# Kernel tuning notes

Measured on AMD Instinct MI355X. Metric: run time of the kernel, lower is better.

The kernel has to match this reference:

```python
import jax, jax.numpy as jnp
import numpy as np

B, T, C, H = 4, 2048, 1024, 16
HS = C // H  # head size = 64

def setup_inputs() -> dict:
    key = jax.random.key(0)
    ks = jax.random.split(key, 3)
    x = jax.random.normal(ks[0], (B, T, C), dtype=jnp.float32)
    w_attn = jax.random.normal(ks[1], (C, 3 * C), dtype=jnp.float32) * (1.0 / np.sqrt(C))
    b_attn = jnp.zeros((3 * C,), dtype=jnp.float32)
    w_proj = jax.random.normal(ks[2], (C, C), dtype=jnp.float32) * (1.0 / np.sqrt(C))
    b_proj = jnp.zeros((C,), dtype=jnp.float32)
    return {"x": x, "w_attn": w_attn, "b_attn": b_attn, "w_proj": w_proj, "b_proj": b_proj}

def reference(x, w_attn, b_attn, w_proj, b_proj):
    b, t, c = x.shape
    qkv = x @ w_attn + b_attn                       # [B,T,3C]
    q, k, v = jnp.split(qkv, 3, axis=2)             # each [B,T,C]
    # [B,T,C] -> [B,H,T,HS]
    q = q.reshape(b, t, H, HS).transpose(0, 2, 1, 3)
    k = k.reshape(b, t, H, HS).transpose(0, 2, 1, 3)
    v = v.reshape(b, t, H, HS).transpose(0, 2, 1, 3)
    scale = 1.0 / np.sqrt(HS)
    att = jnp.einsum('bhqd,bhkd->bhqk', q, k) * scale   # [B,H,T,T]
    causal = jnp.tril(jnp.ones((t, t), dtype=bool))
    att = jnp.where(causal[None, None, :, :], att, -jnp.inf)
    att = jax.nn.softmax(att, axis=-1)
    y = jnp.einsum('bhqk,bhkd->bhqd', att, v)           # [B,H,T,HS]
    y = y.transpose(0, 2, 1, 3).reshape(b, t, c)        # [B,T,C]
    return y @ w_proj + b_proj
```

## Files before the change

### kernel.cpp

```cpp
#include <hip/hip_runtime.h>
#include <hip/hip_bf16.h>

#define B_ 4
#define T_ 2048
#define C_ 1024
#define H_ 16
#define HS_ 64
#define M_ (B_*T_)
#define QSCALE 0.18033688011112042f

typedef __bf16 bf16_t;
typedef bf16_t bf16x8 __attribute__((ext_vector_type(8)));
typedef float f32x4 __attribute__((ext_vector_type(4)));
typedef unsigned short ushort_t;

__device__ __forceinline__ unsigned short f2bf(float f) {
    __hip_bfloat16 h = __float2bfloat16(f);
    return __builtin_bit_cast(unsigned short, h);
}

__device__ __forceinline__ void glds16(const void* g, void* l) {
    __builtin_amdgcn_global_load_lds((const __attribute__((address_space(1))) void*)g,
                                     (__attribute__((address_space(3))) void*)l, 16, 0, 0);
}

__launch_bounds__(256)
__global__ void cvt_x(const float* __restrict__ in, ushort_t* __restrict__ out) {
    int i = blockIdx.x * 256 + threadIdx.x;
    const float4* p = (const float4*)in;
    float4 a = p[i * 2], b = p[i * 2 + 1];
    ushort4 o0, o1;
    o0.x = f2bf(a.x); o0.y = f2bf(a.y); o0.z = f2bf(a.z); o0.w = f2bf(a.w);
    o1.x = f2bf(b.x); o1.y = f2bf(b.y); o1.z = f2bf(b.z); o1.w = f2bf(b.w);
    *(ushort4*)&out[i * 8] = o0;
    *(ushort4*)&out[i * 8 + 4] = o1;
}

__launch_bounds__(256)
__global__ void transpose_cvt(const float* __restrict__ w, ushort_t* __restrict__ wT,
                              int K, int N) {
    __shared__ ushort_t Ts[64][72];
    const int n0 = blockIdx.x * 64, k0 = blockIdx.y * 64;
    const int t = threadIdx.x, r = t >> 2, cq = t & 3;
    #pragma unroll
    for (int j = 0; j < 4; j++) {
        float4 v = *(const float4*)&w[(size_t)(k0 + r) * N + n0 + cq * 16 + j * 4];
        ushort4 o;
        o.x = f2bf(v.x); o.y = f2bf(v.y); o.z = f2bf(v.z); o.w = f2bf(v.w);
        *(ushort4*)&Ts[r][cq * 16 + j * 4] = o;
    }
    __syncthreads();
    #pragma unroll
    for (int j = 0; j < 4; j++) {
        ushort4 o;
        o.x = Ts[cq * 16 + j * 4 + 0][r];
        o.y = Ts[cq * 16 + j * 4 + 1][r];
        o.z = Ts[cq * 16 + j * 4 + 2][r];
        o.w = Ts[cq * 16 + j * 4 + 3][r];
        *(ushort4*)&wT[(size_t)(n0 + r) * K + k0 + cq * 16 + j * 4] = o;
    }
}

__launch_bounds__(256)
__global__ void qkv_gemm(const ushort_t* __restrict__ xb, const ushort_t* __restrict__ wT,
                         const float* __restrict__ bias,
                         ushort_t* __restrict__ qw, ushort_t* __restrict__ kw,
                         ushort_t* __restrict__ vt) {
    const int K = C_;
    __shared__ ushort_t As[2][128 * 32];
    __shared__ ushort_t Bs[2][128 * 32];
    const int tid = threadIdx.x, lane = tid & 63, wid = tid >> 6;
    const int cl = lane & 15, gl = lane >> 4;
    const int waveM = wid >> 1, waveN = wid & 1;
    const int m0 = blockIdx.y * 128, n0 = blockIdx.x * 128;
    const int srow = tid >> 2, scq = tid & 3;
    const int gsw = scq ^ ((srow >> 1) & 3);
    const int asw = 8 * (gl ^ ((cl >> 1) & 3));

    f32x4 acc[4][4];
    #pragma unroll
    for (int mf = 0; mf < 4; mf++)
        #pragma unroll
        for (int nf = 0; nf < 4; nf++) acc[mf][nf] = (f32x4)0.0f;

    #pragma unroll
    for (int i = 0; i < 2; i++) {
        int row = srow + i * 64;
        glds16(&xb[(size_t)(m0 + row) * K + gsw * 8], &As[0][row * 32 + scq * 8]);
        glds16(&wT[(size_t)(n0 + row) * K + gsw * 8], &Bs[0][row * 32 + scq * 8]);
    }
    __syncthreads();

    int cur = 0;
    for (int kk = 0; kk < K; kk += 32) {
        if (kk + 32 < K) {
            #pragma unroll
            for (int i = 0; i < 2; i++) {
                int row = srow + i * 64;
                glds16(&xb[(size_t)(m0 + row) * K + kk + 32 + gsw * 8], &As[cur ^ 1][row * 32 + scq * 8]);
                glds16(&wT[(size_t)(n0 + row) * K + kk + 32 + gsw * 8], &Bs[cur ^ 1][row * 32 + scq * 8]);
            }
        }
        bf16x8 a[4], b[4];
        #pragma unroll
        for (int mf = 0; mf < 4; mf++)
            a[mf] = *(bf16x8*)&As[cur][(waveM * 64 + mf * 16 + cl) * 32 + asw];
        #pragma unroll
        for (int nf = 0; nf < 4; nf++)
            b[nf] = *(bf16x8*)&Bs[cur][(waveN * 64 + nf * 16 + cl) * 32 + asw];
        #pragma unroll
        for (int mf = 0; mf < 4; mf++)
            #pragma unroll
            for (int nf = 0; nf < 4; nf++)
                acc[mf][nf] = __builtin_amdgcn_mfma_f32_16x16x32_bf16(a[mf], b[nf], acc[mf][nf], 0, 0, 0);
        __syncthreads();
        cur ^= 1;
    }
    const int secb = n0 >> 10;
    #pragma unroll
    for (int mf = 0; mf < 4; mf++)
        #pragma unroll
        for (int nf = 0; nf < 4; nf++)
            #pragma unroll
            for (int r = 0; r < 4; r++) {
                int rg = m0 + waveM * 64 + mf * 16 + 4 * gl + r;
                int cg = n0 + waveN * 64 + nf * 16 + cl;
                float val = acc[mf][nf][r] + bias[cg];
                int cc = cg & 1023;
                int h = cc >> 6, hs = cc & 63;
                int bb = rg >> 11, tq = rg & 2047;
                if (secb == 0)
                    qw[(((size_t)(bb * H_ + h)) * T_ + tq) * HS_ + hs] = f2bf(val * QSCALE);
                else if (secb == 1)
                    kw[(((size_t)(bb * H_ + h)) * T_ + tq) * HS_ + hs] = f2bf(val);
                else
                    vt[(((size_t)(bb * H_ + h)) * HS_ + hs) * T_ + tq] = f2bf(val);
            }
}

__launch_bounds__(512, 4)
__global__ void attn_mfma(const ushort_t* __restrict__ qw,
                          const ushort_t* __restrict__ kw,
                          const ushort_t* __restrict__ vt,
                          ushort_t* __restrict__ yw) {
    __shared__ ushort_t Ks[128][72];
    __shared__ ushort_t Vts[64][136];
    __shared__ ushort_t Ps[8][16][136];
    const int tid = threadIdx.x, lane = tid & 63, wid = tid >> 6;
    const int cl = lane & 15, gl = lane >> 4;
    const int qp = blockIdx.x;
    const int bh = blockIdx.y;
    const size_t base = (size_t)bh * T_ * HS_;
    const int bq = bh >> 4, h = bh & 15;
    const int srow = tid >> 3, scq = tid & 7;

    for (int half = 0; half < 2; half++) {
        const int qt = half ? (15 - qp) : qp;
        const int q0 = qt * 128 + wid * 16;
        const int ntiles = qt + 1;

        bf16x8 qf[2];
        #pragma unroll
        for (int kh = 0; kh < 2; kh++)
            qf[kh] = *(const bf16x8*)&qw[base + (size_t)(q0 + cl) * HS_ + kh * 32 + 8 * gl];

        f32x4 o_acc[4];
        #pragma unroll
        for (int dn = 0; dn < 4; dn++) o_acc[dn] = (f32x4)0.0f;
        float m_ = -INFINITY, l_ = 0.f;

        bf16x8 kpre[2], vpre[2], knew[2], vnew[2];
        kpre[0] = *(const bf16x8*)&kw[base + (size_t)srow * HS_ + scq * 8];
        kpre[1] = *(const bf16x8*)&kw[base + (size_t)(64 + srow) * HS_ + scq * 8];
        vpre[0] = *(const bf16x8*)&vt[base + (size_t)srow * T_ + scq * 8];
        vpre[1] = *(const bf16x8*)&vt[base + (size_t)srow * T_ + 64 + scq * 8];

        for (int kt = 0; kt < ntiles; kt++) {
            __syncthreads();
            if (kt + 1 < ntiles) {
                knew[0] = *(const bf16x8*)&kw[base + (size_t)((kt + 1) * 128 + srow) * HS_ + scq * 8];
                knew[1] = *(const bf16x8*)&kw[base + (size_t)((kt + 1) * 128 + 64 + srow) * HS_ + scq * 8];
                vnew[0] = *(const bf16x8*)&vt[base + (size_t)srow * T_ + (kt + 1) * 128 + scq * 8];
                vnew[1] = *(const bf16x8*)&vt[base + (size_t)srow * T_ + (kt + 1) * 128 + 64 + scq * 8];
            }
            *(bf16x8*)&Ks[srow][scq * 8] = kpre[0];
            *(bf16x8*)&Ks[64 + srow][scq * 8] = kpre[1];
            *(bf16x8*)&Vts[srow][scq * 8] = vpre[0];
            *(bf16x8*)&Vts[srow][scq * 8 + 64] = vpre[1];
            __syncthreads();

            {
                const bool full = (kt * 128 + 127 <= q0);

                f32x4 st[8];
                #pragma unroll
                for (int kn = 0; kn < 8; kn++) {
                    bf16x8 kf0 = *(bf16x8*)&Ks[kn * 16 + cl][8 * gl];
                    bf16x8 kf1 = *(bf16x8*)&Ks[kn * 16 + cl][32 + 8 * gl];
                    f32x4 t0 = (f32x4)0.0f;
                    t0 = __builtin_amdgcn_mfma_f32_16x16x32_bf16(kf0, qf[0], t0, 0, 0, 0);
                    st[kn] = __builtin_amdgcn_mfma_f32_16x16x32_bf16(kf1, qf[1], t0, 0, 0, 0);
                }
                if (!full) {
                    const int qg = q0 + cl;
                    #pragma unroll
                    for (int kn = 0; kn < 8; kn++)
                        #pragma unroll
                        for (int r = 0; r < 4; r++) {
                            int kv = kt * 128 + kn * 16 + 4 * gl + r;
                            if (kv > qg) st[kn][r] = -INFINITY;
                        }
                }

                float pmax = st[0][0];
                #pragma unroll
                for (int kn = 0; kn < 8; kn++)
                    #pragma unroll
                    for (int r = 0; r < 4; r++) pmax = fmaxf(pmax, st[kn][r]);
                if (!__all(pmax <= m_ + 8.0f)) {
                    float mx = pmax;
                    mx = fmaxf(mx, __shfl_xor(mx, 16));
                    mx = fmaxf(mx, __shfl_xor(mx, 32));
                    float nm = fmaxf(m_, mx);
                    float al = exp2f(m_ - nm);
                    l_ *= al;
                    #pragma unroll
                    for (int r = 0; r < 4; r++) {
                        float ag = __shfl(al, 4 * gl + r);
                        #pragma unroll
                        for (int dn = 0; dn < 4; dn++) o_acc[dn][r] *= ag;
                    }
                    m_ = nm;
                }

                float ps = 0.f;
                #pragma unroll
                for (int kn = 0; kn < 8; kn++) {
                    float p0 = exp2f(st[kn][0] - m_);
                    float p1 = exp2f(st[kn][1] - m_);
                    float p2 = exp2f(st[kn][2] - m_);
                    float p3 = exp2f(st[kn][3] - m_);
                    ps += (p0 + p1) + (p2 + p3);
                    unsigned lo, hi;
                    asm("v_cvt_pk_bf16_f32 %0, %1, %2" : "=v"(lo) : "v"(p0), "v"(p1));
                    asm("v_cvt_pk_bf16_f32 %0, %1, %2" : "=v"(hi) : "v"(p2), "v"(p3));
                    uint2 wv; wv.x = lo; wv.y = hi;
                    *(uint2*)&Ps[wid][cl][kn * 16 + 4 * gl] = wv;
                }
                l_ += ps;

                bf16x8 pf[4];
                #pragma unroll
                for (int ks = 0; ks < 4; ks++)
                    pf[ks] = *(bf16x8*)&Ps[wid][cl][ks * 32 + 8 * gl];
                #pragma unroll
                for (int dn = 0; dn < 4; dn++)
                    #pragma unroll
                    for (int ks = 0; ks < 4; ks++) {
                        bf16x8 vf = *(bf16x8*)&Vts[dn * 16 + cl][ks * 32 + 8 * gl];
                        o_acc[dn] = __builtin_amdgcn_mfma_f32_16x16x32_bf16(pf[ks], vf, o_acc[dn], 0, 0, 0);
                    }
            }
            #pragma unroll
            for (int i = 0; i < 2; i++) { kpre[i] = knew[i]; vpre[i] = vnew[i]; }
        }

        float ls = l_;
        ls += __shfl_xor(ls, 16);
        ls += __shfl_xor(ls, 32);
        float linv = 1.0f / ls;
        #pragma unroll
        for (int r = 0; r < 4; r++) {
            float lr = __shfl(linv, 4 * gl + r);
            int qg = q0 + 4 * gl + r;
            #pragma unroll
            for (int dn = 0; dn < 4; dn++) {
                int d = dn * 16 + cl;
                yw[((size_t)(bq * T_ + qg)) * C_ + h * HS_ + d] = f2bf(o_acc[dn][r] * lr);
            }
        }
    }
}

__launch_bounds__(256)
__global__ void proj_gemm(const ushort_t* __restrict__ y, const ushort_t* __restrict__ wT,
                          const float* __restrict__ bias, float* __restrict__ out) {
    const int K = C_, N = C_;
    __shared__ ushort_t As[2][128 * 32];
    __shared__ ushort_t Bs[2][128 * 32];
    const int tid = threadIdx.x, lane = tid & 63, wid = tid >> 6;
    const int cl = lane & 15, gl = lane >> 4;
    const int waveM = wid >> 1, waveN = wid & 1;
    const int m0 = blockIdx.y * 128, n0 = blockIdx.x * 128;
    const int srow = tid >> 2, scq = tid & 3;
    const int gsw = scq ^ ((srow >> 1) & 3);
    const int asw = 8 * (gl ^ ((cl >> 1) & 3));

    f32x4 acc[4][4];
    #pragma unroll
    for (int mf = 0; mf < 4; mf++)
        #pragma unroll
        for (int nf = 0; nf < 4; nf++) acc[mf][nf] = (f32x4)0.0f;

    #pragma unroll
    for (int i = 0; i < 2; i++) {
        int row = srow + i * 64;
        glds16(&y[(size_t)(m0 + row) * K + gsw * 8], &As[0][row * 32 + scq * 8]);
        glds16(&wT[(size_t)(n0 + row) * K + gsw * 8], &Bs[0][row * 32 + scq * 8]);
    }
    __syncthreads();

    int cur = 0;
    for (int kk = 0; kk < K; kk += 32) {
        if (kk + 32 < K) {
            #pragma unroll
            for (int i = 0; i < 2; i++) {
                int row = srow + i * 64;
                glds16(&y[(size_t)(m0 + row) * K + kk + 32 + gsw * 8], &As[cur ^ 1][row * 32 + scq * 8]);
                glds16(&wT[(size_t)(n0 + row) * K + kk + 32 + gsw * 8], &Bs[cur ^ 1][row * 32 + scq * 8]);
            }
        }
        bf16x8 a[4], b[4];
        #pragma unroll
        for (int mf = 0; mf < 4; mf++)
            a[mf] = *(bf16x8*)&As[cur][(waveM * 64 + mf * 16 + cl) * 32 + asw];
        #pragma unroll
        for (int nf = 0; nf < 4; nf++)
            b[nf] = *(bf16x8*)&Bs[cur][(waveN * 64 + nf * 16 + cl) * 32 + asw];
        #pragma unroll
        for (int mf = 0; mf < 4; mf++)
            #pragma unroll
            for (int nf = 0; nf < 4; nf++)
                acc[mf][nf] = __builtin_amdgcn_mfma_f32_16x16x32_bf16(a[mf], b[nf], acc[mf][nf], 0, 0, 0);
        __syncthreads();
        cur ^= 1;
    }
    #pragma unroll
    for (int mf = 0; mf < 4; mf++)
        #pragma unroll
        for (int nf = 0; nf < 4; nf++)
            #pragma unroll
            for (int r = 0; r < 4; r++) {
                int rg = m0 + waveM * 64 + mf * 16 + 4 * gl + r;
                int cg = n0 + waveN * 64 + nf * 16 + cl;
                out[(size_t)rg * N + cg] = acc[mf][nf][r] + bias[cg];
            }
}

extern "C" void kernel_launch(void* const* d_in, const int* in_sizes, int n_in,
                              void* d_out, int out_size, void* d_ws, size_t ws_size,
                              hipStream_t stream) {
    const float* x      = (const float*)d_in[0];
    const float* w_attn = (const float*)d_in[1];
    const float* b_attn = (const float*)d_in[2];
    const float* w_proj = (const float*)d_in[3];
    const float* b_proj = (const float*)d_in[4];
    float* out = (float*)d_out;

    const size_t E = (size_t)M_ * C_;
    ushort_t* qw  = (ushort_t*)d_ws;
    ushort_t* kw  = qw + E;
    ushort_t* vt  = kw + E;
    ushort_t* xy  = vt + E;
    ushort_t* wat = xy + E;
    ushort_t* wpt = vt;

    cvt_x<<<dim3(4096), 256, 0, stream>>>(x, xy);
    transpose_cvt<<<dim3(48, 16), 256, 0, stream>>>(w_attn, wat, C_, 3 * C_);
    qkv_gemm<<<dim3(24, 64), 256, 0, stream>>>(xy, wat, b_attn, qw, kw, vt);
    attn_mfma<<<dim3(8, 64), 512, 0, stream>>>(qw, kw, vt, xy);
    transpose_cvt<<<dim3(16, 16), 256, 0, stream>>>(w_proj, wpt, C_, C_);
    proj_gemm<<<dim3(8, 64), 256, 0, stream>>>(xy, wpt, b_proj, out);
}
```

Baseline: 297.7 us.

## Triple-buffer GEMM k-loop with vmcnt waits, swizzle block order, prioritize attention MFMAs

```diff
diff --git a/kernel.cpp b/kernel.cpp
--- a/kernel.cpp
+++ b/kernel.cpp
@@ -67,12 +67,15 @@
                          ushort_t* __restrict__ qw, ushort_t* __restrict__ kw,
                          ushort_t* __restrict__ vt) {
     const int K = C_;
-    __shared__ ushort_t As[2][128 * 32];
-    __shared__ ushort_t Bs[2][128 * 32];
+    __shared__ ushort_t As[3][128 * 32];
+    __shared__ ushort_t Bs[3][128 * 32];
     const int tid = threadIdx.x, lane = tid & 63, wid = tid >> 6;
     const int cl = lane & 15, gl = lane >> 4;
     const int waveM = wid >> 1, waveN = wid & 1;
-    const int m0 = blockIdx.y * 128, n0 = blockIdx.x * 128;
+    const int bid = blockIdx.x;
+    const int swz = (bid & 7) * 192 + (bid >> 3);
+    const int by = swz / 24, bx = swz - by * 24;
+    const int m0 = by * 128, n0 = bx * 128;
     const int srow = tid >> 2, scq = tid & 3;
     const int gsw = scq ^ ((srow >> 1) & 3);
     const int asw = 8 * (gl ^ ((cl >> 1) & 3));
@@ -83,38 +86,38 @@
         #pragma unroll
         for (int nf = 0; nf < 4; nf++) acc[mf][nf] = (f32x4)0.0f;
 
-    #pragma unroll
-    for (int i = 0; i < 2; i++) {
-        int row = srow + i * 64;
-        glds16(&xb[(size_t)(m0 + row) * K + gsw * 8], &As[0][row * 32 + scq * 8]);
-        glds16(&wT[(size_t)(n0 + row) * K + gsw * 8], &Bs[0][row * 32 + scq * 8]);
-    }
-    __syncthreads();
-
-    int cur = 0;
-    for (int kk = 0; kk < K; kk += 32) {
-        if (kk + 32 < K) {
-            #pragma unroll
-            for (int i = 0; i < 2; i++) {
-                int row = srow + i * 64;
-                glds16(&xb[(size_t)(m0 + row) * K + kk + 32 + gsw * 8], &As[cur ^ 1][row * 32 + scq * 8]);
-                glds16(&wT[(size_t)(n0 + row) * K + kk + 32 + gsw * 8], &Bs[cur ^ 1][row * 32 + scq * 8]);
-            }
+    auto stage = [&](int t, int b) {
+        const size_t koff = (size_t)t * 32 + gsw * 8;
+        glds16(&xb[(size_t)(m0 + srow) * K + koff],      &As[b][srow * 32 + scq * 8]);
+        glds16(&xb[(size_t)(m0 + srow + 64) * K + koff], &As[b][(srow + 64) * 32 + scq * 8]);
+        glds16(&wT[(size_t)(n0 + srow) * K + koff],      &Bs[b][srow * 32 + scq * 8]);
+        glds16(&wT[(size_t)(n0 + srow + 64) * K + koff], &Bs[b][(srow + 64) * 32 + scq * 8]);
+    };
+    stage(0, 0);
+    stage(1, 1);
+
+    int bk = 0;
+    for (int ks = 0; ks < 32; ks++) {
+        if (ks < 31) asm volatile("s_waitcnt vmcnt(4)" ::: "memory");
+        else         asm volatile("s_waitcnt vmcnt(0)" ::: "memory");
+        __builtin_amdgcn_s_barrier();
+        if (ks + 2 < 32) {
+            int b2 = bk + 2; if (b2 >= 3) b2 -= 3;
+            stage(ks + 2, b2);
         }
         bf16x8 a[4], b[4];
         #pragma unroll
         for (int mf = 0; mf < 4; mf++)
-            a[mf] = *(bf16x8*)&As[cur][(waveM * 64 + mf * 16 + cl) * 32 + asw];
+            a[mf] = *(bf16x8*)&As[bk][(waveM * 64 + mf * 16 + cl) * 32 + asw];
         #pragma unroll
         for (int nf = 0; nf < 4; nf++)
-            b[nf] = *(bf16x8*)&Bs[cur][(waveN * 64 + nf * 16 + cl) * 32 + asw];
+            b[nf] = *(bf16x8*)&Bs[bk][(waveN * 64 + nf * 16 + cl) * 32 + asw];
         #pragma unroll
         for (int mf = 0; mf < 4; mf++)
             #pragma unroll
             for (int nf = 0; nf < 4; nf++)
                 acc[mf][nf] = __builtin_amdgcn_mfma_f32_16x16x32_bf16(a[mf], b[nf], acc[mf][nf], 0, 0, 0);
-        __syncthreads();
-        cur ^= 1;
+        bk = (bk == 2) ? 0 : bk + 1;
     }
     const int secb = n0 >> 10;
     #pragma unroll
@@ -193,6 +196,7 @@
                 const bool full = (kt * 128 + 127 <= q0);
 
                 f32x4 st[8];
+                __builtin_amdgcn_s_setprio(1);
                 #pragma unroll
                 for (int kn = 0; kn < 8; kn++) {
                     bf16x8 kf0 = *(bf16x8*)&Ks[kn * 16 + cl][8 * gl];
@@ -201,6 +205,7 @@
                     t0 = __builtin_amdgcn_mfma_f32_16x16x32_bf16(kf0, qf[0], t0, 0, 0, 0);
                     st[kn] = __builtin_amdgcn_mfma_f32_16x16x32_bf16(kf1, qf[1], t0, 0, 0, 0);
                 }
+                __builtin_amdgcn_s_setprio(0);
                 if (!full) {
                     const int qg = q0 + cl;
                     #pragma unroll
@@ -253,6 +258,7 @@
                 #pragma unroll
                 for (int ks = 0; ks < 4; ks++)
                     pf[ks] = *(bf16x8*)&Ps[wid][cl][ks * 32 + 8 * gl];
+                __builtin_amdgcn_s_setprio(1);
                 #pragma unroll
                 for (int dn = 0; dn < 4; dn++)
                     #pragma unroll
@@ -260,6 +266,7 @@
                         bf16x8 vf = *(bf16x8*)&Vts[dn * 16 + cl][ks * 32 + 8 * gl];
                         o_acc[dn] = __builtin_amdgcn_mfma_f32_16x16x32_bf16(pf[ks], vf, o_acc[dn], 0, 0, 0);
                     }
+                __builtin_amdgcn_s_setprio(0);
             }
             #pragma unroll
             for (int i = 0; i < 2; i++) { kpre[i] = knew[i]; vpre[i] = vnew[i]; }
@@ -286,12 +293,15 @@
 __global__ void proj_gemm(const ushort_t* __restrict__ y, const ushort_t* __restrict__ wT,
                           const float* __restrict__ bias, float* __restrict__ out) {
     const int K = C_, N = C_;
-    __shared__ ushort_t As[2][128 * 32];
-    __shared__ ushort_t Bs[2][128 * 32];
+    __shared__ ushort_t As[3][128 * 32];
+    __shared__ ushort_t Bs[3][128 * 32];
     const int tid = threadIdx.x, lane = tid & 63, wid = tid >> 6;
     const int cl = lane & 15, gl = lane >> 4;
     const int waveM = wid >> 1, waveN = wid & 1;
-    const int m0 = blockIdx.y * 128, n0 = blockIdx.x * 128;
+    const int bid = blockIdx.x;
+    const int swz = (bid & 7) * 64 + (bid >> 3);
+    const int bx = swz & 7, by = swz >> 3;
+    const int m0 = by * 128, n0 = bx * 128;
     const int srow = tid >> 2, scq = tid & 3;
     const int gsw = scq ^ ((srow >> 1) & 3);
     const int asw = 8 * (gl ^ ((cl >> 1) & 3));
@@ -302,38 +312,38 @@
         #pragma unroll
         for (int nf = 0; nf < 4; nf++) acc[mf][nf] = (f32x4)0.0f;
 
-    #pragma unroll
-    for (int i = 0; i < 2; i++) {
-        int row = srow + i * 64;
-        glds16(&y[(size_t)(m0 + row) * K + gsw * 8], &As[0][row * 32 + scq * 8]);
-        glds16(&wT[(size_t)(n0 + row) * K + gsw * 8], &Bs[0][row * 32 + scq * 8]);
-    }
-    __syncthreads();
-
-    int cur = 0;
-    for (int kk = 0; kk < K; kk += 32) {
-        if (kk + 32 < K) {
-            #pragma unroll
-            for (int i = 0; i < 2; i++) {
-                int row = srow + i * 64;
-                glds16(&y[(size_t)(m0 + row) * K + kk + 32 + gsw * 8], &As[cur ^ 1][row * 32 + scq * 8]);
-                glds16(&wT[(size_t)(n0 + row) * K + kk + 32 + gsw * 8], &Bs[cur ^ 1][row * 32 + scq * 8]);
-            }
+    auto stage = [&](int t, int b) {
+        const size_t koff = (size_t)t * 32 + gsw * 8;
+        glds16(&y[(size_t)(m0 + srow) * K + koff],       &As[b][srow * 32 + scq * 8]);
+        glds16(&y[(size_t)(m0 + srow + 64) * K + koff],  &As[b][(srow + 64) * 32 + scq * 8]);
+        glds16(&wT[(size_t)(n0 + srow) * K + koff],      &Bs[b][srow * 32 + scq * 8]);
+        glds16(&wT[(size_t)(n0 + srow + 64) * K + koff], &Bs[b][(srow + 64) * 32 + scq * 8]);
+    };
+    stage(0, 0);
+    stage(1, 1);
+
+    int bk = 0;
+    for (int ks = 0; ks < 32; ks++) {
+        if (ks < 31) asm volatile("s_waitcnt vmcnt(4)" ::: "memory");
+        else         asm volatile("s_waitcnt vmcnt(0)" ::: "memory");
+        __builtin_amdgcn_s_barrier();
+        if (ks + 2 < 32) {
+            int b2 = bk + 2; if (b2 >= 3) b2 -= 3;
+            stage(ks + 2, b2);
         }
         bf16x8 a[4], b[4];
         #pragma unroll
         for (int mf = 0; mf < 4; mf++)
-            a[mf] = *(bf16x8*)&As[cur][(waveM * 64 + mf * 16 + cl) * 32 + asw];
+            a[mf] = *(bf16x8*)&As[bk][(waveM * 64 + mf * 16 + cl) * 32 + asw];
         #pragma unroll
         for (int nf = 0; nf < 4; nf++)
-            b[nf] = *(bf16x8*)&Bs[cur][(waveN * 64 + nf * 16 + cl) * 32 + asw];
+            b[nf] = *(bf16x8*)&Bs[bk][(waveN * 64 + nf * 16 + cl) * 32 + asw];
         #pragma unroll
         for (int mf = 0; mf < 4; mf++)
             #pragma unroll
             for (int nf = 0; nf < 4; nf++)
                 acc[mf][nf] = __builtin_amdgcn_mfma_f32_16x16x32_bf16(a[mf], b[nf], acc[mf][nf], 0, 0, 0);
-        __syncthreads();
-        cur ^= 1;
+        bk = (bk == 2) ? 0 : bk + 1;
     }
     #pragma unroll
     for (int mf = 0; mf < 4; mf++)
@@ -367,8 +377,8 @@
 
     cvt_x<<<dim3(4096), 256, 0, stream>>>(x, xy);
     transpose_cvt<<<dim3(48, 16), 256, 0, stream>>>(w_attn, wat, C_, 3 * C_);
-    qkv_gemm<<<dim3(24, 64), 256, 0, stream>>>(xy, wat, b_attn, qw, kw, vt);
+    qkv_gemm<<<dim3(1536), 256, 0, stream>>>(xy, wat, b_attn, qw, kw, vt);
     attn_mfma<<<dim3(8, 64), 512, 0, stream>>>(qw, kw, vt, xy);
     transpose_cvt<<<dim3(16, 16), 256, 0, stream>>>(w_proj, wpt, C_, C_);
-    proj_gemm<<<dim3(8, 64), 256, 0, stream>>>(xy, wpt, b_proj, out);
-}
+    proj_gemm<<<dim3(512), 256, 0, stream>>>(xy, wpt, b_proj, out);
+}
```

New measurement: 293.0 us. Within noise of the previous version (-1.6%).
